# Kernel optimization log

Measured on AMD Instinct MI355X. Metric: run time of the kernel, lower is better.

The kernel has to match this reference:

```python
import jax, jax.numpy as jnp
import numpy as np

B, D = 64, 65536   # batch, num default boxes
NEG_POS = 3        # negative:positive mining ratio (init arg)


def _bce_with_logits(x, t):
    # numerically stable elementwise BCE-with-logits (matches torch)
    return jnp.maximum(x, 0.0) - x * t + jnp.log1p(jnp.exp(-jnp.abs(x)))


def _smooth_l1(d):
    ad = jnp.abs(d)
    return jnp.where(ad < 1.0, 0.5 * d * d, ad - 0.5)


def setup_inputs() -> dict:
    key = jax.random.key(0)
    k1, k2, k3, k4 = jax.random.split(key, 4)
    loc_data = jax.random.normal(k1, (B, D, 4), dtype=jnp.float32)
    conf_data = jax.random.normal(k2, (B, D, 1), dtype=jnp.float32)
    loc_t = jax.random.normal(k3, (B, D, 4), dtype=jnp.float32)
    conf_t = (jax.random.uniform(k4, (B, D)) < 0.02).astype(jnp.int32)
    return {"loc_data": loc_data, "conf_data": conf_data,
            "loc_t": loc_t, "conf_t": conf_t}


def reference(loc_data, conf_data, loc_t, conf_t):
    pos = conf_t > 0                                  # [B, D]
    num_pos = pos.sum(axis=1, keepdims=True)          # [B, 1]

    # ---- localization loss: smooth-L1 mean over positive box coords ----
    pf = pos[:, :, None].astype(loc_data.dtype)       # [B, D, 1]
    sl1 = _smooth_l1(loc_data - loc_t) * pf           # [B, D, 4]
    n_loc_elems = pf.sum() * 4.0                      # masked-gather -> mean
    loss_l = sl1.sum() / n_loc_elems

    # ---- confidence loss with hard negative mining ----
    logits = conf_data[:, :, 0]                       # [B, D]
    bce = _bce_with_logits(logits, conf_t.astype(logits.dtype))
    bce_neg = jnp.where(pos, 0.0, bce)                # zero-out positives
    # double argsort -> per-row rank of each element's loss (descending)
    loss_idx = jnp.argsort(-bce_neg, axis=1)          # [B, D]
    idx_rank = jnp.argsort(loss_idx, axis=1)          # [B, D]
    num_neg = jnp.minimum(num_pos * NEG_POS, D)       # [B, 1]
    neg = idx_rank < num_neg                          # top-k hardest negatives
    sel = (pos | neg).astype(logits.dtype)            # [B, D]
    loss_c = (bce * sel).sum() / sel.sum()            # mean over selected

    N = num_pos.sum().astype(logits.dtype)
    return (loss_l / N, loss_c / N)
```

## Files before the change

kernel.cpp:

```cpp
#include <hip/hip_runtime.h>
#include <stdint.h>


#define B_ 64
#define D_ 65536
#define NEGPOS 3
#define BPR 16
#define NBLK (B_ * BPR)
#define CHUNK (D_ / BPR)
#define XC 1.25f
#define LCAP 8192
#define HBINS 4096
#define XRANGE 5.0f
#define CJCAP 1024

#define OFF_SL1P     0
#define OFF_BCEP     8192
#define OFF_NP       16384
#define OFF_CC       20480
#define OFF_NEGSUM   24576
#define OFF_KSEL     25088
#define OFF_CAND     32768

__device__ __forceinline__ float softplus_f(float x) {
    return fmaxf(x, 0.0f) + log1pf(expf(-fabsf(x)));
}

__device__ __forceinline__ int bin_of_x(float x) {
    int b = (int)((x - XC) * ((float)HBINS / XRANGE));
    return max(0, min(HBINS - 1, b));
}

__device__ __forceinline__ float smooth_l1_4(float4 a, float4 b) {
    float s = 0.0f, d, ad;
    d = a.x - b.x; ad = fabsf(d); s += (ad < 1.0f) ? 0.5f * d * d : ad - 0.5f;
    d = a.y - b.y; ad = fabsf(d); s += (ad < 1.0f) ? 0.5f * d * d : ad - 0.5f;
    d = a.z - b.z; ad = fabsf(d); s += (ad < 1.0f) ? 0.5f * d * d : ad - 0.5f;
    d = a.w - b.w; ad = fabsf(d); s += (ad < 1.0f) ? 0.5f * d * d : ad - 0.5f;
    return s;
}

__device__ __forceinline__ double wredD(double v) {
#pragma unroll
    for (int o = 32; o > 0; o >>= 1) v += __shfl_down(v, o, 64);
    return v;
}
__device__ __forceinline__ int wredI(int v) {
#pragma unroll
    for (int o = 32; o > 0; o >>= 1) v += __shfl_down(v, o, 64);
    return v;
}

__global__ void __launch_bounds__(256)
mbl_k1(const float4* __restrict__ loc4, const float* __restrict__ conf,
       const float4* __restrict__ loct4, const int* __restrict__ conft,
       unsigned char* __restrict__ ws)
{
    __shared__ float lcand[CHUNK];
    __shared__ unsigned short lpos[CHUNK];
    __shared__ unsigned wtot[4];
    __shared__ double wr[8];

    const int block = blockIdx.x;
    const int base = block * CHUNK;
    const float4* c4 = (const float4*)(conf + base);
    const int4*   t4 = (const int4*)(conft + base);
    const int lane = threadIdx.x & 63, wid = threadIdx.x >> 6;

    float4 xv[4]; int4 tv[4];
#pragma unroll
    for (int it = 0; it < 4; it++) {
        const int g = threadIdx.x + it * 256;
        xv[it] = c4[g];
        tv[it] = t4[g];
    }

    double bcep = 0.0;
    unsigned cntc = 0, cntp = 0;
#pragma unroll
    for (int it = 0; it < 4; it++) {
#pragma unroll
        for (int c = 0; c < 4; c++) {
            float x = (c == 0) ? xv[it].x : (c == 1) ? xv[it].y : (c == 2) ? xv[it].z : xv[it].w;
            int   t = (c == 0) ? tv[it].x : (c == 1) ? tv[it].y : (c == 2) ? tv[it].z : tv[it].w;
            if (t > 0) { cntp++; bcep += (double)(softplus_f(x) - x); }
            else if (x >= XC) cntc++;
        }
    }

    unsigned pk = (cntc << 16) | cntp;
    unsigned incl = pk;
#pragma unroll
    for (int o = 1; o < 64; o <<= 1) {
        unsigned v = __shfl_up(incl, o, 64);
        if (lane >= o) incl += v;
    }
    unsigned excl = incl - pk;
    if (lane == 63) wtot[wid] = incl;
    __syncthreads();
    unsigned wbase = 0;
    for (int w = 0; w < wid; w++) wbase += wtot[w];
    const unsigned tot = wtot[0] + wtot[1] + wtot[2] + wtot[3];
    const unsigned totc = tot >> 16, totp = tot & 0xFFFFu;
    unsigned offc = (excl >> 16) + (wbase >> 16);
    unsigned offp = (excl & 0xFFFFu) + (wbase & 0xFFFFu);

#pragma unroll
    for (int it = 0; it < 4; it++) {
#pragma unroll
        for (int c = 0; c < 4; c++) {
            float x = (c == 0) ? xv[it].x : (c == 1) ? xv[it].y : (c == 2) ? xv[it].z : xv[it].w;
            int   t = (c == 0) ? tv[it].x : (c == 1) ? tv[it].y : (c == 2) ? tv[it].z : tv[it].w;
            const int li = (threadIdx.x + it * 256) * 4 + c;
            if (t > 0) lpos[offp++] = (unsigned short)li;
            else if (x >= XC) lcand[offc++] = x;
        }
    }
    __syncthreads();

    float* seg = (float*)(ws + OFF_CAND) + (size_t)block * CHUNK;
    for (unsigned i = threadIdx.x; i < totc; i += 256) seg[i] = lcand[i];

    double sl1 = 0.0;
    for (unsigned i = threadIdx.x; i < totp; i += 256) {
        const int e = base + (int)lpos[i];
        sl1 += (double)smooth_l1_4(loc4[e], loct4[e]);
    }

    double s1 = wredD(sl1), s2 = wredD(bcep);
    if (lane == 0) { wr[wid] = s1; wr[4 + wid] = s2; }
    __syncthreads();
    if (threadIdx.x == 0) {
        ((double*)(ws + OFF_SL1P))[block] = wr[0] + wr[1] + wr[2] + wr[3];
        ((double*)(ws + OFF_BCEP))[block] = wr[4] + wr[5] + wr[6] + wr[7];
        ((unsigned*)(ws + OFF_NP))[block] = totp;
        ((unsigned*)(ws + OFF_CC))[block] = totc;
    }
}

__device__ __forceinline__ int blockSumI(int v, int* sh) {
    int w = wredI(v);
    const int lane = threadIdx.x & 63, wid = threadIdx.x >> 6;
    __syncthreads();
    if (lane == 0) sh[wid] = w;
    __syncthreads();
    return sh[0] + sh[1] + sh[2] + sh[3];
}

__global__ void __launch_bounds__(256)
mbl_ksel(const float* __restrict__ conf, const int* __restrict__ conft,
         unsigned char* __restrict__ ws)
{
    __shared__ float lval[LCAP];
    __shared__ unsigned hist[HBINS];
    __shared__ unsigned part[256];
    __shared__ unsigned ubuf[CJCAP];
    __shared__ unsigned segoff[BPR + 1];
    __shared__ unsigned scc[BPR];
    __shared__ unsigned wsuf[4];
    __shared__ unsigned shJ, shRemJ, shCj, shNP;
    __shared__ float shXT;
    __shared__ int shI[4];
    __shared__ double wr[4];

    const int row = blockIdx.x;
    const unsigned* cc = (const unsigned*)(ws + OFF_CC) + row * BPR;
    const unsigned* npb = (const unsigned*)(ws + OFF_NP) + row * BPR;
    const int lane = threadIdx.x & 63, wid = threadIdx.x >> 6;

    if (wid == 0) {
        unsigned c = (lane < BPR) ? cc[lane] : 0u;
        unsigned p = (lane < BPR) ? npb[lane] : 0u;
        unsigned inc = c;
#pragma unroll
        for (int o = 1; o < BPR; o <<= 1) {
            unsigned v = __shfl_up(inc, o, 64);
            if (lane >= o) inc += v;
        }
        unsigned ptot = p;
#pragma unroll
        for (int o = 1; o < BPR; o <<= 1) ptot += __shfl_down(ptot, o, 64);
        if (lane < BPR) { segoff[lane] = inc - c; scc[lane] = c; }
        if (lane == BPR - 1) segoff[BPR] = inc;
        if (lane == 0) { shNP = ptot; shCj = 0; }
    }
    __syncthreads();

    const int np = (int)shNP;
    const unsigned n = segoff[BPR];
    long long k = (long long)np * NEGPOS;
    if (k > D_) k = D_;
    long long negs = (long long)D_ - np;
    if (k > negs) k = negs;
    if (threadIdx.x == 0) ((int*)(ws + OFF_KSEL))[row] = (int)k;
    if (k <= 0) {
        if (threadIdx.x == 0) ((double*)(ws + OFF_NEGSUM))[row] = 0.0;
        return;
    }

    const float* cand = (const float*)(ws + OFF_CAND);
    const float* rowc = conf + row * D_;
    const int*   rowt = conft + row * D_;
    const bool fb = ((long long)n < k) || (n > (unsigned)LCAP);
    float xT;
    int rem;

    if (!fb) {
        {
            const int s = threadIdx.x >> 4, li = threadIdx.x & 15;
            const float* gseg = cand + (size_t)(row * BPR + s) * CHUNK;
            const unsigned cs = scc[s], d0 = segoff[s];
            for (unsigned i = li; i < cs; i += 16) lval[d0 + i] = gseg[i];
        }
        for (int i = threadIdx.x; i < HBINS; i += 256) hist[i] = 0;
        __syncthreads();
        for (unsigned i = threadIdx.x; i < n; i += 256)
            atomicAdd(&hist[bin_of_x(lval[i])], 1u);
        __syncthreads();

        {
            unsigned s = 0; const int b0 = threadIdx.x * 16;
#pragma unroll
            for (int i = 0; i < 16; i++) s += hist[b0 + i];
            part[threadIdx.x] = s;
            unsigned suf = s;
#pragma unroll
            for (int o = 1; o < 64; o <<= 1) {
                unsigned v = __shfl_down(suf, o, 64);
                if (lane + o < 64) suf += v;
            }
            if (lane == 0) wsuf[wid] = suf;
            __syncthreads();
            unsigned add = 0;
            for (int w = wid + 1; w < 4; w++) add += wsuf[w];
            suf += add;
            const unsigned sufx = suf - s;
            if ((long long)sufx < k && (long long)suf >= k) {
                long long cum = sufx;
                for (int b = threadIdx.x * 16 + 15; b >= threadIdx.x * 16; b--) {
                    cum += hist[b];
                    if (cum >= k) {
                        shJ = (unsigned)b;
                        shRemJ = (unsigned)(k - (cum - (long long)hist[b]));
                        break;
                    }
                }
            }
        }
        __syncthreads();
        const unsigned J = shJ, remJ = shRemJ;

        for (unsigned i = threadIdx.x; i < n; i += 256) {
            float x = lval[i];
            if ((unsigned)bin_of_x(x) == J) {
                unsigned p = atomicAdd(&shCj, 1u);
                if (p < CJCAP) ubuf[p] = __float_as_uint(x);
            }
        }
        __syncthreads();
        const unsigned cj = shCj;

        if (cj <= CJCAP) {
            for (unsigned i = threadIdx.x; i < cj; i += 256) {
                const float xi = __uint_as_float(ubuf[i]);
                unsigned gt = 0, ge = 0;
                for (unsigned l = 0; l < cj; l++) {
                    const float xl = __uint_as_float(ubuf[l]);
                    gt += (xl > xi) ? 1u : 0u;
                    ge += (xl >= xi) ? 1u : 0u;
                }
                if (gt < remJ && ge >= remJ) shXT = xi;
            }
            __syncthreads();
            xT = shXT;
        } else {
            float flo = XC - 1.0f, fhi = XC + XRANGE + 1.0f;
            for (int it = 0; it < 40; it++) {
                const float mid = 0.5f * (flo + fhi);
                int c = 0;
                for (unsigned i = threadIdx.x; i < n; i += 256)
                    if (lval[i] > mid) c++;
                const int tot = blockSumI(c, shI);
                if ((long long)tot >= k) flo = mid; else fhi = mid;
                if (!(flo < fhi)) break;
            }
            xT = fhi;
        }

        int c = 0;
        double acc = 0.0;
        for (unsigned i = threadIdx.x; i < n; i += 256) {
            float x = lval[i];
            if (x > xT) { c++; acc += (double)softplus_f(x); }
        }
        const int tot = blockSumI(c, shI);
        rem = (int)(k - (long long)tot);
        double t = wredD(acc);
        if (lane == 0) wr[wid] = t;
        __syncthreads();
        if (threadIdx.x == 0)
            ((double*)(ws + OFF_NEGSUM))[row] =
                wr[0] + wr[1] + wr[2] + wr[3] +
                (double)rem * (double)softplus_f(xT);
    } else {
        unsigned lo = 0u, hi = 0xFFFFFFFFu;
        for (int it = 0; it < 32; it++) {
            const unsigned mid = lo + ((hi - lo) >> 1);
            unsigned um = (mid & 0x80000000u) ? (mid & 0x7FFFFFFFu) : ~mid;
            float fm = __uint_as_float(um);
            int c = 0;
            for (int i = threadIdx.x; i < D_; i += 256)
                if (rowt[i] <= 0 && rowc[i] > fm) c++;
            const int tot = blockSumI(c, shI);
            if ((long long)tot >= k) lo = mid; else hi = mid;
        }
        unsigned uT = (hi & 0x80000000u) ? (hi & 0x7FFFFFFFu) : ~hi;
        xT = __uint_as_float(uT);
        int c = 0;
        double acc = 0.0;
        for (int i = threadIdx.x; i < D_; i += 256) {
            if (rowt[i] <= 0) {
                float x = rowc[i];
                if (x > xT) { c++; acc += (double)softplus_f(x); }
            }
        }
        rem = (int)(k - (long long)blockSumI(c, shI));
        double t = wredD(acc);
        if (lane == 0) wr[wid] = t;
        __syncthreads();
        if (threadIdx.x == 0)
            ((double*)(ws + OFF_NEGSUM))[row] =
                wr[0] + wr[1] + wr[2] + wr[3] +
                (double)rem * (double)softplus_f(xT);
    }
}

__global__ void __launch_bounds__(256)
mbl_k5(unsigned char* __restrict__ ws, float* __restrict__ out)
{
    __shared__ double wrA[4], wrB[4], wrC[4];
    __shared__ int shN[4], shK[4];
    const double* sl1p = (const double*)(ws + OFF_SL1P);
    const double* bcep = (const double*)(ws + OFF_BCEP);
    const unsigned* npb = (const unsigned*)(ws + OFF_NP);
    const int* ksel = (const int*)(ws + OFF_KSEL);
    const double* ns = (const double*)(ws + OFF_NEGSUM);

    double a = 0.0, b = 0.0, c = 0.0;
    int n = 0, kk = 0;
    for (int i = threadIdx.x; i < NBLK; i += 256) {
        a += sl1p[i]; b += bcep[i]; n += (int)npb[i];
    }
    if (threadIdx.x < 64) { kk = ksel[threadIdx.x]; c = ns[threadIdx.x]; }

    double ra = wredD(a), rb = wredD(b), rc = wredD(c);
    int rn = wredI(n), rk = wredI(kk);
    const int lane = threadIdx.x & 63, wid = threadIdx.x >> 6;
    if (lane == 0) { wrA[wid] = ra; wrB[wid] = rb; wrC[wid] = rc; shN[wid] = rn; shK[wid] = rk; }
    __syncthreads();
    if (threadIdx.x == 0) {
        double SL1 = wrA[0] + wrA[1] + wrA[2] + wrA[3];
        double BCE = wrB[0] + wrB[1] + wrB[2] + wrB[3];
        double NSUM = wrC[0] + wrC[1] + wrC[2] + wrC[3];
        double Np = (double)(shN[0] + shN[1] + shN[2] + shN[3]);
        double Kt = (double)(shK[0] + shK[1] + shK[2] + shK[3]);
        double out0 = (Np > 0.0) ? (SL1 / (4.0 * Np)) / Np : 0.0;
        double denom = Np + Kt;
        double out1 = (Np > 0.0 && denom > 0.0) ? ((BCE + NSUM) / denom) / Np : 0.0;
        out[0] = (float)out0;
        out[1] = (float)out1;
    }
}

extern "C" void kernel_launch(void* const* d_in, const int* in_sizes, int n_in,
                              void* d_out, int out_size, void* d_ws, size_t ws_size,
                              hipStream_t stream)
{
    const float4* loc4  = (const float4*)d_in[0];
    const float*  conf  = (const float*)d_in[1];
    const float4* loct4 = (const float4*)d_in[2];
    const int*    conft = (const int*)d_in[3];
    unsigned char* ws = (unsigned char*)d_ws;
    float* out = (float*)d_out;

    mbl_k1<<<dim3(NBLK), dim3(256), 0, stream>>>(loc4, conf, loct4, conft, ws);
    mbl_ksel<<<dim3(B_), dim3(256), 0, stream>>>(conf, conft, ws);
    mbl_k5<<<dim3(1), dim3(256), 0, stream>>>(ws, out);
}
```

Before: 174.8 us.

## Fuse three kernels into one using last-block-done atomic counters

```diff
diff --git a/kernel.cpp b/kernel.cpp
--- a/kernel.cpp
+++ b/kernel.cpp
@@ -9,17 +9,20 @@
 #define NBLK (B_ * BPR)
 #define CHUNK (D_ / BPR)
 #define XC 1.25f
-#define LCAP 8192
+#define CAPR 16384
 #define HBINS 4096
 #define XRANGE 5.0f
 #define CJCAP 1024
 
-#define OFF_SL1P     0
-#define OFF_BCEP     8192
-#define OFF_NP       16384
-#define OFF_CC       20480
-#define OFF_NEGSUM   24576
-#define OFF_KSEL     25088
+#define OFF_CANDCNT  0
+#define OFF_NPROW    256
+#define OFF_ROWDONE  512
+#define OFF_ALLDONE  768
+#define ZERO_BYTES   1024
+#define OFF_SL1P     1024
+#define OFF_BCEP     9216
+#define OFF_NEGSUM   17408
+#define OFF_KSEL     17920
 #define OFF_CAND     32768
 
 __device__ __forceinline__ float softplus_f(float x) {
@@ -29,6 +32,15 @@
 __device__ __forceinline__ int bin_of_x(float x) {
     int b = (int)((x - XC) * ((float)HBINS / XRANGE));
     return max(0, min(HBINS - 1, b));
+}
+
+__device__ __forceinline__ unsigned sortkey(float x) {
+    unsigned u = __float_as_uint(x);
+    return (u & 0x80000000u) ? ~u : (u | 0x80000000u);
+}
+__device__ __forceinline__ float unsortkey(unsigned s) {
+    unsigned u = (s & 0x80000000u) ? (s & 0x7FFFFFFFu) : ~s;
+    return __uint_as_float(u);
 }
 
 __device__ __forceinline__ float smooth_l1_4(float4 a, float4 b) {
@@ -51,324 +63,310 @@
     return v;
 }
 
+union ShUnion {
+    struct { float lcand[CHUNK]; unsigned short lpos[CHUNK]; } a;
+    struct { unsigned hist[HBINS]; unsigned ubuf[CJCAP]; } b;
+};
+
 __global__ void __launch_bounds__(256)
-mbl_k1(const float4* __restrict__ loc4, const float* __restrict__ conf,
-       const float4* __restrict__ loct4, const int* __restrict__ conft,
-       unsigned char* __restrict__ ws)
+mbl_fused(const float4* __restrict__ loc4, const float* __restrict__ conf,
+          const float4* __restrict__ loct4, const int* __restrict__ conft,
+          unsigned char* __restrict__ ws, float* __restrict__ out)
 {
-    __shared__ float lcand[CHUNK];
-    __shared__ unsigned short lpos[CHUNK];
-    __shared__ unsigned wtot[4];
-    __shared__ double wr[8];
+    __shared__ ShUnion sh;
+    __shared__ unsigned wtot[4], wsuf[4];
+    __shared__ unsigned shSel, shBase, shJ, shRemJ, shCj, shWin;
+    __shared__ float shXT;
+    __shared__ int shI[4], shN[4], shK[4];
+    __shared__ double wr[8], wrC[4];
 
     const int block = blockIdx.x;
+    const int row = block / BPR;
     const int base = block * CHUNK;
-    const float4* c4 = (const float4*)(conf + base);
-    const int4*   t4 = (const int4*)(conft + base);
     const int lane = threadIdx.x & 63, wid = threadIdx.x >> 6;
-
-    float4 xv[4]; int4 tv[4];
-#pragma unroll
-    for (int it = 0; it < 4; it++) {
-        const int g = threadIdx.x + it * 256;
-        xv[it] = c4[g];
-        tv[it] = t4[g];
+    const int tid = threadIdx.x;
+
+    unsigned* candcnt = (unsigned*)(ws + OFF_CANDCNT);
+    unsigned* nprow   = (unsigned*)(ws + OFF_NPROW);
+    unsigned* rowdone = (unsigned*)(ws + OFF_ROWDONE);
+    unsigned* alldone = (unsigned*)(ws + OFF_ALLDONE);
+    double*   sl1p    = (double*)(ws + OFF_SL1P);
+    double*   bcepp   = (double*)(ws + OFF_BCEP);
+    double*   negsum  = (double*)(ws + OFF_NEGSUM);
+    int*      kselp   = (int*)(ws + OFF_KSEL);
+    float*    cand    = (float*)(ws + OFF_CAND);
+
+    {
+        const float4* c4 = (const float4*)(conf + base);
+        const int4*   t4 = (const int4*)(conft + base);
+        float4 xv[4]; int4 tv[4];
+#pragma unroll
+        for (int it = 0; it < 4; it++) {
+            const int g = tid + it * 256;
+            xv[it] = c4[g];
+            tv[it] = t4[g];
+        }
+
+        double bcep = 0.0;
+        unsigned cntc = 0, cntp = 0;
+#pragma unroll
+        for (int it = 0; it < 4; it++) {
+#pragma unroll
+            for (int c = 0; c < 4; c++) {
+                float x = (c == 0) ? xv[it].x : (c == 1) ? xv[it].y : (c == 2) ? xv[it].z : xv[it].w;
+                int   t = (c == 0) ? tv[it].x : (c == 1) ? tv[it].y : (c == 2) ? tv[it].z : tv[it].w;
+                if (t > 0) { cntp++; bcep += (double)(softplus_f(x) - x); }
+                else if (x >= XC) cntc++;
+            }
+        }
+
+        unsigned pk = (cntc << 16) | cntp;
+        unsigned incl = pk;
+#pragma unroll
+        for (int o = 1; o < 64; o <<= 1) {
+            unsigned v = __shfl_up(incl, o, 64);
+            if (lane >= o) incl += v;
+        }
+        unsigned excl = incl - pk;
+        if (lane == 63) wtot[wid] = incl;
+        __syncthreads();
+        unsigned wbase = 0;
+        for (int w = 0; w < wid; w++) wbase += wtot[w];
+        const unsigned tot = wtot[0] + wtot[1] + wtot[2] + wtot[3];
+        const unsigned totc = tot >> 16, totp = tot & 0xFFFFu;
+        unsigned offc = (excl >> 16) + (wbase >> 16);
+        unsigned offp = (excl & 0xFFFFu) + (wbase & 0xFFFFu);
+
+#pragma unroll
+        for (int it = 0; it < 4; it++) {
+#pragma unroll
+            for (int c = 0; c < 4; c++) {
+                float x = (c == 0) ? xv[it].x : (c == 1) ? xv[it].y : (c == 2) ? xv[it].z : xv[it].w;
+                int   t = (c == 0) ? tv[it].x : (c == 1) ? tv[it].y : (c == 2) ? tv[it].z : tv[it].w;
+                const int li = (tid + it * 256) * 4 + c;
+                if (t > 0) sh.a.lpos[offp++] = (unsigned short)li;
+                else if (x >= XC) sh.a.lcand[offc++] = x;
+            }
+        }
+        __syncthreads();
+
+        if (tid == 0) {
+            shBase = atomicAdd(&candcnt[row], totc);
+            if (totp) atomicAdd(&nprow[row], totp);
+        }
+        __syncthreads();
+        {
+            float* crow = cand + (size_t)row * CAPR;
+            const unsigned b0 = shBase;
+            for (unsigned i = tid; i < totc; i += 256) {
+                unsigned p = b0 + i;
+                if (p < CAPR) crow[p] = sh.a.lcand[i];
+            }
+        }
+
+        double sl1 = 0.0;
+        for (unsigned i = tid; i < totp; i += 256) {
+            const int e = base + (int)sh.a.lpos[i];
+            sl1 += (double)smooth_l1_4(loc4[e], loct4[e]);
+        }
+
+        double s1 = wredD(sl1), s2 = wredD(bcep);
+        if (lane == 0) { wr[wid] = s1; wr[4 + wid] = s2; }
+        __syncthreads();
+        if (tid == 0) {
+            sl1p[block]  = wr[0] + wr[1] + wr[2] + wr[3];
+            bcepp[block] = wr[4] + wr[5] + wr[6] + wr[7];
+        }
     }
 
-    double bcep = 0.0;
-    unsigned cntc = 0, cntp = 0;
-#pragma unroll
-    for (int it = 0; it < 4; it++) {
-#pragma unroll
-        for (int c = 0; c < 4; c++) {
-            float x = (c == 0) ? xv[it].x : (c == 1) ? xv[it].y : (c == 2) ? xv[it].z : xv[it].w;
-            int   t = (c == 0) ? tv[it].x : (c == 1) ? tv[it].y : (c == 2) ? tv[it].z : tv[it].w;
-            if (t > 0) { cntp++; bcep += (double)(softplus_f(x) - x); }
-            else if (x >= XC) cntc++;
-        }
-    }
-
-    unsigned pk = (cntc << 16) | cntp;
-    unsigned incl = pk;
-#pragma unroll
-    for (int o = 1; o < 64; o <<= 1) {
-        unsigned v = __shfl_up(incl, o, 64);
-        if (lane >= o) incl += v;
-    }
-    unsigned excl = incl - pk;
-    if (lane == 63) wtot[wid] = incl;
+    __threadfence();
     __syncthreads();
-    unsigned wbase = 0;
-    for (int w = 0; w < wid; w++) wbase += wtot[w];
-    const unsigned tot = wtot[0] + wtot[1] + wtot[2] + wtot[3];
-    const unsigned totc = tot >> 16, totp = tot & 0xFFFFu;
-    unsigned offc = (excl >> 16) + (wbase >> 16);
-    unsigned offp = (excl & 0xFFFFu) + (wbase & 0xFFFFu);
-
-#pragma unroll
-    for (int it = 0; it < 4; it++) {
-#pragma unroll
-        for (int c = 0; c < 4; c++) {
-            float x = (c == 0) ? xv[it].x : (c == 1) ? xv[it].y : (c == 2) ? xv[it].z : xv[it].w;
-            int   t = (c == 0) ? tv[it].x : (c == 1) ? tv[it].y : (c == 2) ? tv[it].z : tv[it].w;
-            const int li = (threadIdx.x + it * 256) * 4 + c;
-            if (t > 0) lpos[offp++] = (unsigned short)li;
-            else if (x >= XC) lcand[offc++] = x;
-        }
-    }
+    if (tid == 0) shSel = atomicAdd(&rowdone[row], 1u);
     __syncthreads();
-
-    float* seg = (float*)(ws + OFF_CAND) + (size_t)block * CHUNK;
-    for (unsigned i = threadIdx.x; i < totc; i += 256) seg[i] = lcand[i];
-
-    double sl1 = 0.0;
-    for (unsigned i = threadIdx.x; i < totp; i += 256) {
-        const int e = base + (int)lpos[i];
-        sl1 += (double)smooth_l1_4(loc4[e], loct4[e]);
-    }
-
-    double s1 = wredD(sl1), s2 = wredD(bcep);
-    if (lane == 0) { wr[wid] = s1; wr[4 + wid] = s2; }
-    __syncthreads();
-    if (threadIdx.x == 0) {
-        ((double*)(ws + OFF_SL1P))[block] = wr[0] + wr[1] + wr[2] + wr[3];
-        ((double*)(ws + OFF_BCEP))[block] = wr[4] + wr[5] + wr[6] + wr[7];
-        ((unsigned*)(ws + OFF_NP))[block] = totp;
-        ((unsigned*)(ws + OFF_CC))[block] = totc;
-    }
-}
-
-__device__ __forceinline__ int blockSumI(int v, int* sh) {
-    int w = wredI(v);
-    const int lane = threadIdx.x & 63, wid = threadIdx.x >> 6;
-    __syncthreads();
-    if (lane == 0) sh[wid] = w;
-    __syncthreads();
-    return sh[0] + sh[1] + sh[2] + sh[3];
-}
-
-__global__ void __launch_bounds__(256)
-mbl_ksel(const float* __restrict__ conf, const int* __restrict__ conft,
-         unsigned char* __restrict__ ws)
-{
-    __shared__ float lval[LCAP];
-    __shared__ unsigned hist[HBINS];
-    __shared__ unsigned part[256];
-    __shared__ unsigned ubuf[CJCAP];
-    __shared__ unsigned segoff[BPR + 1];
-    __shared__ unsigned scc[BPR];
-    __shared__ unsigned wsuf[4];
-    __shared__ unsigned shJ, shRemJ, shCj, shNP;
-    __shared__ float shXT;
-    __shared__ int shI[4];
-    __shared__ double wr[4];
-
-    const int row = blockIdx.x;
-    const unsigned* cc = (const unsigned*)(ws + OFF_CC) + row * BPR;
-    const unsigned* npb = (const unsigned*)(ws + OFF_NP) + row * BPR;
-    const int lane = threadIdx.x & 63, wid = threadIdx.x >> 6;
-
-    if (wid == 0) {
-        unsigned c = (lane < BPR) ? cc[lane] : 0u;
-        unsigned p = (lane < BPR) ? npb[lane] : 0u;
-        unsigned inc = c;
-#pragma unroll
-        for (int o = 1; o < BPR; o <<= 1) {
-            unsigned v = __shfl_up(inc, o, 64);
-            if (lane >= o) inc += v;
-        }
-        unsigned ptot = p;
-#pragma unroll
-        for (int o = 1; o < BPR; o <<= 1) ptot += __shfl_down(ptot, o, 64);
-        if (lane < BPR) { segoff[lane] = inc - c; scc[lane] = c; }
-        if (lane == BPR - 1) segoff[BPR] = inc;
-        if (lane == 0) { shNP = ptot; shCj = 0; }
-    }
-    __syncthreads();
-
-    const int np = (int)shNP;
-    const unsigned n = segoff[BPR];
+    if (shSel != BPR - 1) return;
+
+    __threadfence();
+    const unsigned n = atomicAdd(&candcnt[row], 0u);
+    const int np = (int)atomicAdd(&nprow[row], 0u);
     long long k = (long long)np * NEGPOS;
     if (k > D_) k = D_;
     long long negs = (long long)D_ - np;
     if (k > negs) k = negs;
-    if (threadIdx.x == 0) ((int*)(ws + OFF_KSEL))[row] = (int)k;
-    if (k <= 0) {
-        if (threadIdx.x == 0) ((double*)(ws + OFF_NEGSUM))[row] = 0.0;
-        return;
-    }
-
-    const float* cand = (const float*)(ws + OFF_CAND);
+
+    const float* crow = cand + (size_t)row * CAPR;
     const float* rowc = conf + row * D_;
     const int*   rowt = conft + row * D_;
-    const bool fb = ((long long)n < k) || (n > (unsigned)LCAP);
-    float xT;
-    int rem;
-
-    if (!fb) {
-        {
-            const int s = threadIdx.x >> 4, li = threadIdx.x & 15;
-            const float* gseg = cand + (size_t)(row * BPR + s) * CHUNK;
-            const unsigned cs = scc[s], d0 = segoff[s];
-            for (unsigned i = li; i < cs; i += 16) lval[d0 + i] = gseg[i];
-        }
-        for (int i = threadIdx.x; i < HBINS; i += 256) hist[i] = 0;
-        __syncthreads();
-        for (unsigned i = threadIdx.x; i < n; i += 256)
-            atomicAdd(&hist[bin_of_x(lval[i])], 1u);
-        __syncthreads();
-
-        {
-            unsigned s = 0; const int b0 = threadIdx.x * 16;
-#pragma unroll
-            for (int i = 0; i < 16; i++) s += hist[b0 + i];
-            part[threadIdx.x] = s;
-            unsigned suf = s;
-#pragma unroll
-            for (int o = 1; o < 64; o <<= 1) {
-                unsigned v = __shfl_down(suf, o, 64);
-                if (lane + o < 64) suf += v;
-            }
-            if (lane == 0) wsuf[wid] = suf;
-            __syncthreads();
-            unsigned add = 0;
-            for (int w = wid + 1; w < 4; w++) add += wsuf[w];
-            suf += add;
-            const unsigned sufx = suf - s;
-            if ((long long)sufx < k && (long long)suf >= k) {
-                long long cum = sufx;
-                for (int b = threadIdx.x * 16 + 15; b >= threadIdx.x * 16; b--) {
-                    cum += hist[b];
-                    if (cum >= k) {
-                        shJ = (unsigned)b;
-                        shRemJ = (unsigned)(k - (cum - (long long)hist[b]));
-                        break;
+    float xT = 0.0f;
+    int rem = 0;
+    double nsum = 0.0;
+
+    if (k > 0) {
+        const bool fb = ((long long)n < k) || (n > (unsigned)CAPR);
+        if (!fb) {
+            for (int i = tid; i < HBINS; i += 256) sh.b.hist[i] = 0;
+            if (tid == 0) shCj = 0;
+            __syncthreads();
+            for (unsigned i = tid; i < n; i += 256)
+                atomicAdd(&sh.b.hist[bin_of_x(crow[i])], 1u);
+            __syncthreads();
+
+            {
+                unsigned s = 0; const int b0 = tid * 16;
+#pragma unroll
+                for (int i = 0; i < 16; i++) s += sh.b.hist[b0 + i];
+                unsigned suf = s;
+#pragma unroll
+                for (int o = 1; o < 64; o <<= 1) {
+                    unsigned v = __shfl_down(suf, o, 64);
+                    if (lane + o < 64) suf += v;
+                }
+                if (lane == 0) wsuf[wid] = suf;
+                __syncthreads();
+                unsigned add = 0;
+                for (int w = wid + 1; w < 4; w++) add += wsuf[w];
+                suf += add;
+                const unsigned sufx = suf - s;
+                if ((long long)sufx < k && (long long)suf >= k) {
+                    long long cum = sufx;
+                    for (int b = tid * 16 + 15; b >= tid * 16; b--) {
+                        cum += sh.b.hist[b];
+                        if (cum >= k) {
+                            shJ = (unsigned)b;
+                            shRemJ = (unsigned)(k - (cum - (long long)sh.b.hist[b]));
+                            break;
+                        }
                     }
                 }
             }
-        }
-        __syncthreads();
-        const unsigned J = shJ, remJ = shRemJ;
-
-        for (unsigned i = threadIdx.x; i < n; i += 256) {
-            float x = lval[i];
-            if ((unsigned)bin_of_x(x) == J) {
-                unsigned p = atomicAdd(&shCj, 1u);
-                if (p < CJCAP) ubuf[p] = __float_as_uint(x);
-            }
-        }
-        __syncthreads();
-        const unsigned cj = shCj;
-
-        if (cj <= CJCAP) {
-            for (unsigned i = threadIdx.x; i < cj; i += 256) {
-                const float xi = __uint_as_float(ubuf[i]);
-                unsigned gt = 0, ge = 0;
-                for (unsigned l = 0; l < cj; l++) {
-                    const float xl = __uint_as_float(ubuf[l]);
-                    gt += (xl > xi) ? 1u : 0u;
-                    ge += (xl >= xi) ? 1u : 0u;
-                }
-                if (gt < remJ && ge >= remJ) shXT = xi;
-            }
-            __syncthreads();
-            xT = shXT;
+            __syncthreads();
+            const unsigned J = shJ, remJ = shRemJ;
+
+            for (unsigned i = tid; i < n; i += 256) {
+                float x = crow[i];
+                if ((unsigned)bin_of_x(x) == J) {
+                    unsigned p = atomicAdd(&shCj, 1u);
+                    if (p < CJCAP) sh.b.ubuf[p] = __float_as_uint(x);
+                }
+            }
+            __syncthreads();
+            const unsigned cj = shCj;
+
+            if (cj <= CJCAP) {
+                for (unsigned i = tid; i < cj; i += 256) {
+                    const float xi = __uint_as_float(sh.b.ubuf[i]);
+                    unsigned gt = 0, ge = 0;
+                    for (unsigned l = 0; l < cj; l++) {
+                        const float xl = __uint_as_float(sh.b.ubuf[l]);
+                        gt += (xl > xi) ? 1u : 0u;
+                        ge += (xl >= xi) ? 1u : 0u;
+                    }
+                    if (gt < remJ && ge >= remJ) shXT = xi;
+                }
+                __syncthreads();
+                xT = shXT;
+            } else {
+                unsigned lo = 0u, hi = 0xFFFFFFFFu;
+                for (int it = 0; it < 32; it++) {
+                    const unsigned mid = lo + ((hi - lo) >> 1);
+                    const float fm = unsortkey(mid);
+                    int c = 0;
+                    for (unsigned i = tid; i < n; i += 256)
+                        if (crow[i] > fm) c++;
+                    int w = wredI(c);
+                    __syncthreads();
+                    if (lane == 0) shI[wid] = w;
+                    __syncthreads();
+                    const int tot = shI[0] + shI[1] + shI[2] + shI[3];
+                    if ((long long)tot >= k) lo = mid; else hi = mid;
+                }
+                xT = unsortkey(hi);
+            }
+
+            int c = 0;
+            double acc = 0.0;
+            for (unsigned i = tid; i < n; i += 256) {
+                float x = crow[i];
+                if (x > xT) { c++; acc += (double)softplus_f(x); }
+            }
+            int w = wredI(c);
+            double t = wredD(acc);
+            __syncthreads();
+            if (lane == 0) { shI[wid] = w; wr[wid] = t; }
+            __syncthreads();
+            rem = (int)(k - (long long)(shI[0] + shI[1] + shI[2] + shI[3]));
+            nsum = wr[0] + wr[1] + wr[2] + wr[3] +
+                   (double)rem * (double)softplus_f(xT);
         } else {
-            float flo = XC - 1.0f, fhi = XC + XRANGE + 1.0f;
-            for (int it = 0; it < 40; it++) {
-                const float mid = 0.5f * (flo + fhi);
+            unsigned lo = 0u, hi = 0xFFFFFFFFu;
+            for (int it = 0; it < 32; it++) {
+                const unsigned mid = lo + ((hi - lo) >> 1);
+                const float fm = unsortkey(mid);
                 int c = 0;
-                for (unsigned i = threadIdx.x; i < n; i += 256)
-                    if (lval[i] > mid) c++;
-                const int tot = blockSumI(c, shI);
-                if ((long long)tot >= k) flo = mid; else fhi = mid;
-                if (!(flo < fhi)) break;
-            }
-            xT = fhi;
-        }
-
-        int c = 0;
-        double acc = 0.0;
-        for (unsigned i = threadIdx.x; i < n; i += 256) {
-            float x = lval[i];
-            if (x > xT) { c++; acc += (double)softplus_f(x); }
-        }
-        const int tot = blockSumI(c, shI);
-        rem = (int)(k - (long long)tot);
-        double t = wredD(acc);
-        if (lane == 0) wr[wid] = t;
-        __syncthreads();
-        if (threadIdx.x == 0)
-            ((double*)(ws + OFF_NEGSUM))[row] =
-                wr[0] + wr[1] + wr[2] + wr[3] +
-                (double)rem * (double)softplus_f(xT);
-    } else {
-        unsigned lo = 0u, hi = 0xFFFFFFFFu;
-        for (int it = 0; it < 32; it++) {
-            const unsigned mid = lo + ((hi - lo) >> 1);
-            unsigned um = (mid & 0x80000000u) ? (mid & 0x7FFFFFFFu) : ~mid;
-            float fm = __uint_as_float(um);
+                for (int i = tid; i < D_; i += 256)
+                    if (rowt[i] <= 0 && rowc[i] > fm) c++;
+                int w = wredI(c);
+                __syncthreads();
+                if (lane == 0) shI[wid] = w;
+                __syncthreads();
+                const int tot = shI[0] + shI[1] + shI[2] + shI[3];
+                if ((long long)tot >= k) lo = mid; else hi = mid;
+            }
+            xT = unsortkey(hi);
             int c = 0;
-            for (int i = threadIdx.x; i < D_; i += 256)
-                if (rowt[i] <= 0 && rowc[i] > fm) c++;
-            const int tot = blockSumI(c, shI);
-            if ((long long)tot >= k) lo = mid; else hi = mid;
-        }
-        unsigned uT = (hi & 0x80000000u) ? (hi & 0x7FFFFFFFu) : ~hi;
-        xT = __uint_as_float(uT);
-        int c = 0;
-        double acc = 0.0;
-        for (int i = threadIdx.x; i < D_; i += 256) {
-            if (rowt[i] <= 0) {
-                float x = rowc[i];
-                if (x > xT) { c++; acc += (double)softplus_f(x); }
-            }
-        }
-        rem = (int)(k - (long long)blockSumI(c, shI));
-        double t = wredD(acc);
-        if (lane == 0) wr[wid] = t;
-        __syncthreads();
-        if (threadIdx.x == 0)
-            ((double*)(ws + OFF_NEGSUM))[row] =
-                wr[0] + wr[1] + wr[2] + wr[3] +
-                (double)rem * (double)softplus_f(xT);
+            double acc = 0.0;
+            for (int i = tid; i < D_; i += 256) {
+                if (rowt[i] <= 0) {
+                    float x = rowc[i];
+                    if (x > xT) { c++; acc += (double)softplus_f(x); }
+                }
+            }
+            int w = wredI(c);
+            double t = wredD(acc);
+            __syncthreads();
+            if (lane == 0) { shI[wid] = w; wr[wid] = t; }
+            __syncthreads();
+            rem = (int)(k - (long long)(shI[0] + shI[1] + shI[2] + shI[3]));
+            nsum = wr[0] + wr[1] + wr[2] + wr[3] +
+                   (double)rem * (double)softplus_f(xT);
+        }
     }
-}
-
-__global__ void __launch_bounds__(256)
-mbl_k5(unsigned char* __restrict__ ws, float* __restrict__ out)
-{
-    __shared__ double wrA[4], wrB[4], wrC[4];
-    __shared__ int shN[4], shK[4];
-    const double* sl1p = (const double*)(ws + OFF_SL1P);
-    const double* bcep = (const double*)(ws + OFF_BCEP);
-    const unsigned* npb = (const unsigned*)(ws + OFF_NP);
-    const int* ksel = (const int*)(ws + OFF_KSEL);
-    const double* ns = (const double*)(ws + OFF_NEGSUM);
-
-    double a = 0.0, b = 0.0, c = 0.0;
-    int n = 0, kk = 0;
-    for (int i = threadIdx.x; i < NBLK; i += 256) {
-        a += sl1p[i]; b += bcep[i]; n += (int)npb[i];
-    }
-    if (threadIdx.x < 64) { kk = ksel[threadIdx.x]; c = ns[threadIdx.x]; }
-
-    double ra = wredD(a), rb = wredD(b), rc = wredD(c);
-    int rn = wredI(n), rk = wredI(kk);
-    const int lane = threadIdx.x & 63, wid = threadIdx.x >> 6;
-    if (lane == 0) { wrA[wid] = ra; wrB[wid] = rb; wrC[wid] = rc; shN[wid] = rn; shK[wid] = rk; }
+
+    if (tid == 0) { negsum[row] = nsum; kselp[row] = (int)k; }
+
+    __threadfence();
     __syncthreads();
-    if (threadIdx.x == 0) {
-        double SL1 = wrA[0] + wrA[1] + wrA[2] + wrA[3];
-        double BCE = wrB[0] + wrB[1] + wrB[2] + wrB[3];
-        double NSUM = wrC[0] + wrC[1] + wrC[2] + wrC[3];
-        double Np = (double)(shN[0] + shN[1] + shN[2] + shN[3]);
-        double Kt = (double)(shK[0] + shK[1] + shK[2] + shK[3]);
-        double out0 = (Np > 0.0) ? (SL1 / (4.0 * Np)) / Np : 0.0;
-        double denom = Np + Kt;
-        double out1 = (Np > 0.0 && denom > 0.0) ? ((BCE + NSUM) / denom) / Np : 0.0;
-        out[0] = (float)out0;
-        out[1] = (float)out1;
+    if (tid == 0) shWin = atomicAdd(alldone, 1u);
+    __syncthreads();
+    if (shWin != B_ - 1) return;
+
+    __threadfence();
+    {
+        double a = 0.0, b = 0.0, c = 0.0;
+        int nn = 0, kk = 0;
+        for (int i = tid; i < NBLK; i += 256) { a += sl1p[i]; b += bcepp[i]; }
+        if (tid < B_) {
+            nn = (int)atomicAdd(&nprow[tid], 0u);
+            kk = kselp[tid];
+            c = negsum[tid];
+        }
+        double ra = wredD(a), rb = wredD(b), rc = wredD(c);
+        int rn = wredI(nn), rk = wredI(kk);
+        __syncthreads();
+        if (lane == 0) { wr[wid] = ra; wr[4 + wid] = rb; wrC[wid] = rc;
+                         shN[wid] = rn; shK[wid] = rk; }
+        __syncthreads();
+        if (tid == 0) {
+            double SL1 = wr[0] + wr[1] + wr[2] + wr[3];
+            double BCE = wr[4] + wr[5] + wr[6] + wr[7];
+            double NSUM = wrC[0] + wrC[1] + wrC[2] + wrC[3];
+            double Np = (double)(shN[0] + shN[1] + shN[2] + shN[3]);
+            double Kt = (double)(shK[0] + shK[1] + shK[2] + shK[3]);
+            double out0 = (Np > 0.0) ? (SL1 / (4.0 * Np)) / Np : 0.0;
+            double denom = Np + Kt;
+            double out1 = (Np > 0.0 && denom > 0.0) ? ((BCE + NSUM) / denom) / Np : 0.0;
+            out[0] = (float)out0;
+            out[1] = (float)out1;
+        }
     }
 }
 
@@ -383,7 +381,6 @@
     unsigned char* ws = (unsigned char*)d_ws;
     float* out = (float*)d_out;
 
-    mbl_k1<<<dim3(NBLK), dim3(256), 0, stream>>>(loc4, conf, loct4, conft, ws);
-    mbl_ksel<<<dim3(B_), dim3(256), 0, stream>>>(conf, conft, ws);
-    mbl_k5<<<dim3(1), dim3(256), 0, stream>>>(ws, out);
-}
+    hipMemsetAsync(ws, 0, ZERO_BYTES, stream);
+    mbl_fused<<<dim3(NBLK), dim3(256), 0, stream>>>(loc4, conf, loct4, conft, ws, out);
+}
```

Result: slower. 331.0 us (+89.4%).

## Build per-block candidate histograms in first pass and select threshold from merged histograms

Applied to the files above, without the earlier changes.

```diff
diff --git a/kernel.cpp b/kernel.cpp
--- a/kernel.cpp
+++ b/kernel.cpp
@@ -9,10 +9,9 @@
 #define NBLK (B_ * BPR)
 #define CHUNK (D_ / BPR)
 #define XC 1.25f
-#define LCAP 8192
-#define HBINS 4096
+#define HBINS 256
 #define XRANGE 5.0f
-#define CJCAP 1024
+#define CJCAP 2048
 
 #define OFF_SL1P     0
 #define OFF_BCEP     8192
@@ -20,7 +19,8 @@
 #define OFF_CC       20480
 #define OFF_NEGSUM   24576
 #define OFF_KSEL     25088
-#define OFF_CAND     32768
+#define OFF_BHIST    32768
+#define OFF_CAND     1081344
 
 __device__ __forceinline__ float softplus_f(float x) {
     return fmaxf(x, 0.0f) + log1pf(expf(-fabsf(x)));
@@ -29,6 +29,11 @@
 __device__ __forceinline__ int bin_of_x(float x) {
     int b = (int)((x - XC) * ((float)HBINS / XRANGE));
     return max(0, min(HBINS - 1, b));
+}
+
+__device__ __forceinline__ float unsortkey(unsigned s) {
+    unsigned u = (s & 0x80000000u) ? (s & 0x7FFFFFFFu) : ~s;
+    return __uint_as_float(u);
 }
 
 __device__ __forceinline__ float smooth_l1_4(float4 a, float4 b) {
@@ -51,6 +56,15 @@
     return v;
 }
 
+__device__ __forceinline__ int blockSumI(int v, int* sh) {
+    int w = wredI(v);
+    const int lane = threadIdx.x & 63, wid = threadIdx.x >> 6;
+    __syncthreads();
+    if (lane == 0) sh[wid] = w;
+    __syncthreads();
+    return sh[0] + sh[1] + sh[2] + sh[3];
+}
+
 __global__ void __launch_bounds__(256)
 mbl_k1(const float4* __restrict__ loc4, const float* __restrict__ conf,
        const float4* __restrict__ loct4, const int* __restrict__ conft,
@@ -58,6 +72,7 @@
 {
     __shared__ float lcand[CHUNK];
     __shared__ unsigned short lpos[CHUNK];
+    __shared__ unsigned lhist[HBINS];
     __shared__ unsigned wtot[4];
     __shared__ double wr[8];
 
@@ -66,14 +81,18 @@
     const float4* c4 = (const float4*)(conf + base);
     const int4*   t4 = (const int4*)(conft + base);
     const int lane = threadIdx.x & 63, wid = threadIdx.x >> 6;
+    const int tid = threadIdx.x;
+
+    lhist[tid] = 0;
 
     float4 xv[4]; int4 tv[4];
 #pragma unroll
     for (int it = 0; it < 4; it++) {
-        const int g = threadIdx.x + it * 256;
+        const int g = tid + it * 256;
         xv[it] = c4[g];
         tv[it] = t4[g];
     }
+    __syncthreads();
 
     double bcep = 0.0;
     unsigned cntc = 0, cntp = 0;
@@ -84,7 +103,7 @@
             float x = (c == 0) ? xv[it].x : (c == 1) ? xv[it].y : (c == 2) ? xv[it].z : xv[it].w;
             int   t = (c == 0) ? tv[it].x : (c == 1) ? tv[it].y : (c == 2) ? tv[it].z : tv[it].w;
             if (t > 0) { cntp++; bcep += (double)(softplus_f(x) - x); }
-            else if (x >= XC) cntc++;
+            else if (x >= XC) { cntc++; atomicAdd(&lhist[bin_of_x(x)], 1u); }
         }
     }
 
@@ -111,7 +130,7 @@
         for (int c = 0; c < 4; c++) {
             float x = (c == 0) ? xv[it].x : (c == 1) ? xv[it].y : (c == 2) ? xv[it].z : xv[it].w;
             int   t = (c == 0) ? tv[it].x : (c == 1) ? tv[it].y : (c == 2) ? tv[it].z : tv[it].w;
-            const int li = (threadIdx.x + it * 256) * 4 + c;
+            const int li = (tid + it * 256) * 4 + c;
             if (t > 0) lpos[offp++] = (unsigned short)li;
             else if (x >= XC) lcand[offc++] = x;
         }
@@ -119,10 +138,11 @@
     __syncthreads();
 
     float* seg = (float*)(ws + OFF_CAND) + (size_t)block * CHUNK;
-    for (unsigned i = threadIdx.x; i < totc; i += 256) seg[i] = lcand[i];
+    for (unsigned i = tid; i < totc; i += 256) seg[i] = lcand[i];
+    ((unsigned*)(ws + OFF_BHIST))[(size_t)block * HBINS + tid] = lhist[tid];
 
     double sl1 = 0.0;
-    for (unsigned i = threadIdx.x; i < totp; i += 256) {
+    for (unsigned i = tid; i < totp; i += 256) {
         const int e = base + (int)lpos[i];
         sl1 += (double)smooth_l1_4(loc4[e], loct4[e]);
     }
@@ -130,7 +150,7 @@
     double s1 = wredD(sl1), s2 = wredD(bcep);
     if (lane == 0) { wr[wid] = s1; wr[4 + wid] = s2; }
     __syncthreads();
-    if (threadIdx.x == 0) {
+    if (tid == 0) {
         ((double*)(ws + OFF_SL1P))[block] = wr[0] + wr[1] + wr[2] + wr[3];
         ((double*)(ws + OFF_BCEP))[block] = wr[4] + wr[5] + wr[6] + wr[7];
         ((unsigned*)(ws + OFF_NP))[block] = totp;
@@ -138,35 +158,22 @@
     }
 }
 
-__device__ __forceinline__ int blockSumI(int v, int* sh) {
-    int w = wredI(v);
-    const int lane = threadIdx.x & 63, wid = threadIdx.x >> 6;
-    __syncthreads();
-    if (lane == 0) sh[wid] = w;
-    __syncthreads();
-    return sh[0] + sh[1] + sh[2] + sh[3];
-}
-
 __global__ void __launch_bounds__(256)
 mbl_ksel(const float* __restrict__ conf, const int* __restrict__ conft,
          unsigned char* __restrict__ ws)
 {
-    __shared__ float lval[LCAP];
-    __shared__ unsigned hist[HBINS];
-    __shared__ unsigned part[256];
+    __shared__ unsigned segoff[BPR + 1], scc[BPR];
+    __shared__ unsigned wsuf[4];
     __shared__ unsigned ubuf[CJCAP];
-    __shared__ unsigned segoff[BPR + 1];
-    __shared__ unsigned scc[BPR];
-    __shared__ unsigned wsuf[4];
     __shared__ unsigned shJ, shRemJ, shCj, shNP;
     __shared__ float shXT;
     __shared__ int shI[4];
     __shared__ double wr[4];
 
     const int row = blockIdx.x;
-    const unsigned* cc = (const unsigned*)(ws + OFF_CC) + row * BPR;
+    const int tid = threadIdx.x, lane = tid & 63, wid = tid >> 6;
+    const unsigned* cc  = (const unsigned*)(ws + OFF_CC) + row * BPR;
     const unsigned* npb = (const unsigned*)(ws + OFF_NP) + row * BPR;
-    const int lane = threadIdx.x & 63, wid = threadIdx.x >> 6;
 
     if (wid == 0) {
         unsigned c = (lane < BPR) ? cc[lane] : 0u;
@@ -182,7 +189,7 @@
         for (int o = 1; o < BPR; o <<= 1) ptot += __shfl_down(ptot, o, 64);
         if (lane < BPR) { segoff[lane] = inc - c; scc[lane] = c; }
         if (lane == BPR - 1) segoff[BPR] = inc;
-        if (lane == 0) { shNP = ptot; shCj = 0; }
+        if (lane == 0) { shNP = ptot; shCj = 0; shJ = 0xFFFFFFFFu; }
     }
     __syncthreads();
 
@@ -192,76 +199,63 @@
     if (k > D_) k = D_;
     long long negs = (long long)D_ - np;
     if (k > negs) k = negs;
-    if (threadIdx.x == 0) ((int*)(ws + OFF_KSEL))[row] = (int)k;
+    if (tid == 0) ((int*)(ws + OFF_KSEL))[row] = (int)k;
     if (k <= 0) {
-        if (threadIdx.x == 0) ((double*)(ws + OFF_NEGSUM))[row] = 0.0;
+        if (tid == 0) ((double*)(ws + OFF_NEGSUM))[row] = 0.0;
         return;
     }
 
     const float* cand = (const float*)(ws + OFF_CAND);
     const float* rowc = conf + row * D_;
     const int*   rowt = conft + row * D_;
-    const bool fb = ((long long)n < k) || (n > (unsigned)LCAP);
-    float xT;
-    int rem;
-
-    if (!fb) {
-        {
-            const int s = threadIdx.x >> 4, li = threadIdx.x & 15;
-            const float* gseg = cand + (size_t)(row * BPR + s) * CHUNK;
-            const unsigned cs = scc[s], d0 = segoff[s];
-            for (unsigned i = li; i < cs; i += 16) lval[d0 + i] = gseg[i];
-        }
-        for (int i = threadIdx.x; i < HBINS; i += 256) hist[i] = 0;
+    float xT = 0.0f;
+    int c = 0;
+    double acc = 0.0;
+
+    if ((long long)n >= k) {
+        const unsigned* bh = (const unsigned*)(ws + OFF_BHIST) +
+                             (size_t)(row * BPR) * HBINS;
+        unsigned h = 0;
+#pragma unroll
+        for (int s = 0; s < BPR; s++) h += bh[s * HBINS + tid];
+
+        unsigned suf = h;
+#pragma unroll
+        for (int o = 1; o < 64; o <<= 1) {
+            unsigned v = __shfl_down(suf, o, 64);
+            if (lane + o < 64) suf += v;
+        }
+        if (lane == 0) wsuf[wid] = suf;
         __syncthreads();
-        for (unsigned i = threadIdx.x; i < n; i += 256)
-            atomicAdd(&hist[bin_of_x(lval[i])], 1u);
-        __syncthreads();
-
-        {
-            unsigned s = 0; const int b0 = threadIdx.x * 16;
-#pragma unroll
-            for (int i = 0; i < 16; i++) s += hist[b0 + i];
-            part[threadIdx.x] = s;
-            unsigned suf = s;
-#pragma unroll
-            for (int o = 1; o < 64; o <<= 1) {
-                unsigned v = __shfl_down(suf, o, 64);
-                if (lane + o < 64) suf += v;
-            }
-            if (lane == 0) wsuf[wid] = suf;
-            __syncthreads();
-            unsigned add = 0;
-            for (int w = wid + 1; w < 4; w++) add += wsuf[w];
-            suf += add;
-            const unsigned sufx = suf - s;
-            if ((long long)sufx < k && (long long)suf >= k) {
-                long long cum = sufx;
-                for (int b = threadIdx.x * 16 + 15; b >= threadIdx.x * 16; b--) {
-                    cum += hist[b];
-                    if (cum >= k) {
-                        shJ = (unsigned)b;
-                        shRemJ = (unsigned)(k - (cum - (long long)hist[b]));
-                        break;
-                    }
-                }
-            }
+        unsigned add = 0;
+        for (int w = wid + 1; w < 4; w++) add += wsuf[w];
+        suf += add;
+        if ((long long)suf >= k && (long long)(suf - h) < k) {
+            shJ = (unsigned)tid;
+            shRemJ = (unsigned)(k - (long long)(suf - h));
         }
         __syncthreads();
         const unsigned J = shJ, remJ = shRemJ;
 
-        for (unsigned i = threadIdx.x; i < n; i += 256) {
-            float x = lval[i];
-            if ((unsigned)bin_of_x(x) == J) {
-                unsigned p = atomicAdd(&shCj, 1u);
-                if (p < CJCAP) ubuf[p] = __float_as_uint(x);
+        {
+            const int s = tid >> 4, li = tid & 15;
+            const float* gseg = cand + (size_t)(row * BPR + s) * CHUNK;
+            const unsigned cs = scc[s];
+            for (unsigned i = li; i < cs; i += 16) {
+                float x = gseg[i];
+                unsigned b = (unsigned)bin_of_x(x);
+                if (b > J) { c++; acc += (double)softplus_f(x); }
+                else if (b == J) {
+                    unsigned p = atomicAdd(&shCj, 1u);
+                    if (p < CJCAP) ubuf[p] = __float_as_uint(x);
+                }
             }
         }
         __syncthreads();
         const unsigned cj = shCj;
 
-        if (cj <= CJCAP) {
-            for (unsigned i = threadIdx.x; i < cj; i += 256) {
+        if (cj <= (unsigned)CJCAP) {
+            for (unsigned i = tid; i < cj; i += 256) {
                 const float xi = __uint_as_float(ubuf[i]);
                 unsigned gt = 0, ge = 0;
                 for (unsigned l = 0; l < cj; l++) {
@@ -273,65 +267,63 @@
             }
             __syncthreads();
             xT = shXT;
+            for (unsigned i = tid; i < cj; i += 256) {
+                const float xi = __uint_as_float(ubuf[i]);
+                if (xi > xT) { c++; acc += (double)softplus_f(xi); }
+            }
         } else {
-            float flo = XC - 1.0f, fhi = XC + XRANGE + 1.0f;
-            for (int it = 0; it < 40; it++) {
-                const float mid = 0.5f * (flo + fhi);
-                int c = 0;
-                for (unsigned i = threadIdx.x; i < n; i += 256)
-                    if (lval[i] > mid) c++;
-                const int tot = blockSumI(c, shI);
-                if ((long long)tot >= k) flo = mid; else fhi = mid;
-                if (!(flo < fhi)) break;
-            }
-            xT = fhi;
-        }
-
-        int c = 0;
-        double acc = 0.0;
-        for (unsigned i = threadIdx.x; i < n; i += 256) {
-            float x = lval[i];
-            if (x > xT) { c++; acc += (double)softplus_f(x); }
-        }
-        const int tot = blockSumI(c, shI);
-        rem = (int)(k - (long long)tot);
-        double t = wredD(acc);
-        if (lane == 0) wr[wid] = t;
-        __syncthreads();
-        if (threadIdx.x == 0)
-            ((double*)(ws + OFF_NEGSUM))[row] =
-                wr[0] + wr[1] + wr[2] + wr[3] +
-                (double)rem * (double)softplus_f(xT);
+            const int s = tid >> 4, li = tid & 15;
+            const float* gseg = cand + (size_t)(row * BPR + s) * CHUNK;
+            const unsigned cs = scc[s];
+            unsigned lo = 0u, hi = 0xFFFFFFFFu;
+            for (int it = 0; it < 32; it++) {
+                const unsigned mid = lo + ((hi - lo) >> 1);
+                const float fm = unsortkey(mid);
+                int c2 = 0;
+                for (unsigned i = li; i < cs; i += 16)
+                    if (gseg[i] > fm) c2++;
+                const int tot = blockSumI(c2, shI);
+                if ((long long)tot >= k) lo = mid; else hi = mid;
+            }
+            xT = unsortkey(hi);
+            c = 0; acc = 0.0;
+            for (unsigned i = li; i < cs; i += 16) {
+                float x = gseg[i];
+                if (x > xT) { c++; acc += (double)softplus_f(x); }
+            }
+        }
     } else {
         unsigned lo = 0u, hi = 0xFFFFFFFFu;
         for (int it = 0; it < 32; it++) {
             const unsigned mid = lo + ((hi - lo) >> 1);
-            unsigned um = (mid & 0x80000000u) ? (mid & 0x7FFFFFFFu) : ~mid;
-            float fm = __uint_as_float(um);
-            int c = 0;
-            for (int i = threadIdx.x; i < D_; i += 256)
-                if (rowt[i] <= 0 && rowc[i] > fm) c++;
-            const int tot = blockSumI(c, shI);
+            const float fm = unsortkey(mid);
+            int c2 = 0;
+            for (int i = tid; i < D_; i += 256)
+                if (rowt[i] <= 0 && rowc[i] > fm) c2++;
+            const int tot = blockSumI(c2, shI);
             if ((long long)tot >= k) lo = mid; else hi = mid;
         }
-        unsigned uT = (hi & 0x80000000u) ? (hi & 0x7FFFFFFFu) : ~hi;
-        xT = __uint_as_float(uT);
-        int c = 0;
-        double acc = 0.0;
-        for (int i = threadIdx.x; i < D_; i += 256) {
+        xT = unsortkey(hi);
+        c = 0; acc = 0.0;
+        for (int i = tid; i < D_; i += 256) {
             if (rowt[i] <= 0) {
                 float x = rowc[i];
                 if (x > xT) { c++; acc += (double)softplus_f(x); }
             }
         }
-        rem = (int)(k - (long long)blockSumI(c, shI));
-        double t = wredD(acc);
-        if (lane == 0) wr[wid] = t;
-        __syncthreads();
-        if (threadIdx.x == 0)
-            ((double*)(ws + OFF_NEGSUM))[row] =
-                wr[0] + wr[1] + wr[2] + wr[3] +
-                (double)rem * (double)softplus_f(xT);
+    }
+
+    int w = wredI(c);
+    double t = wredD(acc);
+    __syncthreads();
+    if (lane == 0) { shI[wid] = w; wr[wid] = t; }
+    __syncthreads();
+    if (tid == 0) {
+        const int tot = shI[0] + shI[1] + shI[2] + shI[3];
+        const int rem = (int)(k - (long long)tot);
+        ((double*)(ws + OFF_NEGSUM))[row] =
+            wr[0] + wr[1] + wr[2] + wr[3] +
+            (double)rem * (double)softplus_f(xT);
     }
 }
 
```

Result: no change. 177.7 us (+1.6%).
